# Kernel optimization log

Hardware: AMD Instinct MI355X
Metric: run time of the kernel (lower is better)

The kernel has to match this reference:

```python
import jax, jax.numpy as jnp
import numpy as np

B, N, C_IN, F, OUT = 32, 1000, 128, 128, 64
RATIOS = (0.8, 0.8)


def setup_inputs() -> dict:
    key = jax.random.key(0)
    ks = jax.random.split(key, 10)
    N_nodes = jax.random.randint(ks[0], (B,), 500, N + 1, dtype=jnp.int32)
    ar = jnp.arange(N)
    mask = (ar[None, :] < N_nodes[:, None]).astype(jnp.float32)  # [B,N]
    A = (jax.random.uniform(ks[1], (B, N, N)) < 0.02).astype(jnp.float32)
    A = A * (1.0 - jnp.eye(N, dtype=jnp.float32))
    A = jnp.maximum(A, A.transpose(0, 2, 1))  # symmetric, no self loops
    A = A * mask[:, :, None] * mask[:, None, :]
    x = jax.random.normal(ks[2], (B, N, C_IN)) * mask[..., None]

    def lin(k, fin, fout):
        bnd = 1.0 / np.sqrt(fin)
        kw, kb = jax.random.split(k)
        W = jax.random.uniform(kw, (fout, fin), minval=-bnd, maxval=bnd)
        b = jax.random.uniform(kb, (fout,), minval=-bnd, maxval=bnd)
        return W, b

    W0, b0 = lin(ks[3], C_IN, F)
    W1, b1 = lin(ks[4], F, F)
    W2, b2 = lin(ks[5], F, F)
    bnd = 1.0 / np.sqrt(F)
    p0 = jax.random.uniform(ks[6], (F, 1), minval=-bnd, maxval=bnd)
    p1 = jax.random.uniform(ks[7], (F, 1), minval=-bnd, maxval=bnd)
    Wfc, bfc = lin(ks[8], F, OUT)
    return dict(x=x, A=A, mask=mask, N_nodes=N_nodes,
                W0=W0, b0=b0, W1=W1, b1=b1, W2=W2, b2=b2,
                p0=p0, p1=p1, Wfc=Wfc, bfc=bfc)


def _gconv(x, A, mask, W, b):
    # K=1 Kipf-Welling conv: L = D^-1/2 (A+I) D^-1/2; relu(Linear(L x)) * mask
    n = A.shape[1]
    A_hat = A + jnp.eye(n, dtype=A.dtype)
    D = (jnp.sum(A_hat, axis=1) + 1e-5) ** -0.5  # [B,N]
    L = D[:, :, None] * A_hat * D[:, None, :]
    h = jnp.einsum('bij,bjc->bic', L, x)
    h = h @ W.T + b
    return jax.nn.relu(h) * mask[..., None]


def _pool(x, A, mask, N_nodes, p, ratio):
    # score each node, drop the N_remove lowest-scoring valid nodes per graph
    y = (x @ p)[..., 0] / jnp.sqrt(jnp.sum(p ** 2))  # [B,N]
    N_remove = (N_nodes.astype(jnp.float32) * (1.0 - ratio)).astype(jnp.int32)
    y_key = jnp.where(mask > 0, y, jnp.inf)  # invalid nodes rank last
    ranks = jnp.argsort(jnp.argsort(y_key, axis=1), axis=1)  # ascending rank
    new_mask = ((ranks >= N_remove[:, None]) & (mask > 0)).astype(x.dtype)
    x = x * jnp.tanh(y)[..., None] * new_mask[..., None]
    A = new_mask[:, :, None] * A * new_mask[:, None, :]
    return x, A, new_mask, N_nodes - N_remove


def reference(x, A, mask, N_nodes, W0, b0, W1, b1, W2, b2, p0, p1, Wfc, bfc):
    h = _gconv(x, A, mask, W0, b0)
    h, A1, m1, n1 = _pool(h, A, mask, N_nodes, p0, RATIOS[0])
    h = _gconv(h, A1, m1, W1, b1)
    h, A2, m2, n2 = _pool(h, A1, m1, n1, p1, RATIOS[1])
    h = _gconv(h, A2, m2, W2, b2)
    g = jnp.max(h, axis=1)  # [B,F] global max pool
    return g @ Wfc.T + bfc  # [B,OUT]
```

## Files before the change

### kernel.cpp

```cpp
#include <hip/hip_runtime.h>
#include <math.h>

#define BB 32
#define NN 1000
#define CC 128
#define FF 128
#define OO 64
#define CAP 128
#define NB 40

#define RMC ((float)(1.0 - 0.8))


__global__ void k_csr(const float* __restrict__ A, const float* __restrict__ mask,
                      const int* __restrict__ Nn,
                      const float* __restrict__ p0, const float* __restrict__ p1,
                      const float* __restrict__ W0, const float* __restrict__ W1,
                      const float* __restrict__ W2,
                      short* __restrict__ idx, int* __restrict__ cnt,
                      float* __restrict__ D, float* __restrict__ dg,
                      float* __restrict__ m, float* __restrict__ gate,
                      int* __restrict__ ncur0, float* __restrict__ pn,
                      float* __restrict__ Wt){
  int blk = blockIdx.x, lane = threadIdx.x;
  int r8 = blk & 7, t = blk >> 3;
  int b = r8 + 8*(t/1001), i = t % 1001;
  if (i == NN){
    for (int j = lane; j < NN; j += 64){
      float v = mask[b*NN + j]; m[b*NN + j] = v; gate[b*NN + j] = v;
    }
    if (lane == 0) ncur0[b] = Nn[b];
    if (b == 0 && lane == 1){ float s=0.f; for(int c=0;c<FF;c++) s += p0[c]*p0[c]; pn[0] = sqrtf(s); }
    if (b == 1 && lane == 1){ float s=0.f; for(int c=0;c<FF;c++) s += p1[c]*p1[c]; pn[1] = sqrtf(s); }
    for (int e = b*1536 + lane; e < (b+1)*1536; e += 64){
      int s = e / (FF*CC), rem = e % (FF*CC);
      int c = rem >> 7, f = rem & 127;
      const float* W = (s == 0) ? W0 : (s == 1) ? W1 : W2;
      Wt[(size_t)s*FF*CC + rem] = W[f*CC + c];
    }
    return;
  }
  if (mask[b*NN + i] == 0.f){
    if (lane == 0){
      cnt[b*NN + i] = 0;
      D[b*NN + i]  = 1.0f / sqrtf(1.0f + 1e-5f);
      dg[b*NN + i] = 0.f;
    }
    return;
  }
  const float4* row = (const float4*)(A + ((size_t)b*NN + i)*NN);
  short* out = idx + ((size_t)b*NN + i)*CAP;
  int count = 0;
  for (int base = 0; base < 250; base += 64){
    int q = base + lane;
    float4 v;
    if (q < 250) v = row[q]; else { v.x=v.y=v.z=v.w=0.f; }
    int lc = (v.x!=0.f) + (v.y!=0.f) + (v.z!=0.f) + (v.w!=0.f);
    int pre = lc;
    #pragma unroll
    for (int off = 1; off < 64; off <<= 1){
      int t2 = __shfl_up(pre, off);
      if (lane >= off) pre += t2;
    }
    int tot = __shfl(pre, 63);
    pre -= lc;
    int slot = count + pre;
    int j = q*4;
    if (v.x!=0.f && slot < CAP) out[slot++] = (short)j;
    if (v.y!=0.f && slot < CAP) out[slot++] = (short)(j+1);
    if (v.z!=0.f && slot < CAP) out[slot++] = (short)(j+2);
    if (v.w!=0.f && slot < CAP) out[slot++] = (short)(j+3);
    count += tot;
  }
  if (lane == 0){
    int cn = (count < CAP) ? count : CAP;
    cnt[b*NN + i] = cn;
    float Dv = 1.0f / sqrtf((float)cn + 1.0f + 1e-5f);
    D[b*NN + i]  = Dv;
    dg[b*NN + i] = Dv;
  }
}

__global__ void k_agglin(const short* __restrict__ idx, const int* __restrict__ cnt,
                         const float* __restrict__ D, const float* __restrict__ dg,
                         const float* __restrict__ m, const float* __restrict__ gate,
                         const float* __restrict__ h,
                         const float* __restrict__ Wt,
                         const float* __restrict__ bias, float* __restrict__ Hout){
  __shared__ float t[NB][CC];
  __shared__ int   nb[8][CAP];
  __shared__ float dn[8][CAP];
  int blk = blockIdx.x, tid = threadIdx.x;
  int r8 = blk & 7, tq = blk >> 3;
  int b = r8 + 8*(tq/25);
  int i0 = (tq % 25) * NB;
  int w = tid >> 6, lane = tid & 63;
  int g = lane >> 5, l32 = lane & 31;
  const float* hb = h + (size_t)b*NN*CC;
  int*   nbw = nb[w];
  float* dnw = dn[w];
  for (int q = 0; q < 5; q++){
    int lr = q*8 + w;
    int i  = i0 + lr;
    if (m[b*NN + i] == 0.f){
      if (g == 0){ float4 z = {0.f,0.f,0.f,0.f}; *(float4*)&t[lr][l32<<2] = z; }
      continue;
    }
    int n = cnt[b*NN + i];
    const short* r = idx + ((size_t)b*NN + i)*CAP;
    int j0 = 0; float d0 = 0.f; bool k0 = false;
    if (lane < n){ j0 = (int)r[lane]; d0 = dg[b*NN + j0]; k0 = (d0 != 0.f); }
    unsigned long long bal = __ballot(k0);
    int pre = __popcll(bal & ((1ull << lane) - 1ull));
    if (k0){ nbw[pre] = j0*CC; dnw[pre] = d0; }
    int nlive = __popcll(bal);
    if (n > 64){
      int e = lane + 64; int j1 = 0; float d1 = 0.f; bool k1 = false;
      if (e < n){ j1 = (int)r[e]; d1 = dg[b*NN + j1]; k1 = (d1 != 0.f); }
      unsigned long long bal1 = __ballot(k1);
      int pre1 = __popcll(bal1 & ((1ull << lane) - 1ull));
      if (k1){ nbw[nlive + pre1] = j1*CC; dnw[nlive + pre1] = d1; }
      nlive += __popcll(bal1);
    }
    int np = (nlive + 15) & ~15;
    if (lane < np - nlive){ nbw[nlive + lane] = 0; dnw[nlive + lane] = 0.f; }
    __builtin_amdgcn_wave_barrier();
    float4 a0 = {0.f,0.f,0.f,0.f}, a1 = a0, a2 = a0, a3 = a0;
    for (int k = 0; k < np; k += 16){
      int e = k + g;
      float4 v0 = *(const float4*)(hb + nbw[e   ] + (l32<<2));
      float4 v1 = *(const float4*)(hb + nbw[e+ 2] + (l32<<2));
      float4 v2 = *(const float4*)(hb + nbw[e+ 4] + (l32<<2));
      float4 v3 = *(const float4*)(hb + nbw[e+ 6] + (l32<<2));
      float4 v4 = *(const float4*)(hb + nbw[e+ 8] + (l32<<2));
      float4 v5 = *(const float4*)(hb + nbw[e+10] + (l32<<2));
      float4 v6 = *(const float4*)(hb + nbw[e+12] + (l32<<2));
      float4 v7 = *(const float4*)(hb + nbw[e+14] + (l32<<2));
      float e0 = dnw[e], e1 = dnw[e+2], e2 = dnw[e+4], e3 = dnw[e+6];
      float e4 = dnw[e+8], e5 = dnw[e+10], e6 = dnw[e+12], e7 = dnw[e+14];
      a0.x += e0*v0.x; a0.y += e0*v0.y; a0.z += e0*v0.z; a0.w += e0*v0.w;
      a1.x += e1*v1.x; a1.y += e1*v1.y; a1.z += e1*v1.z; a1.w += e1*v1.w;
      a2.x += e2*v2.x; a2.y += e2*v2.y; a2.z += e2*v2.z; a2.w += e2*v2.w;
      a3.x += e3*v3.x; a3.y += e3*v3.y; a3.z += e3*v3.z; a3.w += e3*v3.w;
      a0.x += e4*v4.x; a0.y += e4*v4.y; a0.z += e4*v4.z; a0.w += e4*v4.w;
      a1.x += e5*v5.x; a1.y += e5*v5.y; a1.z += e5*v5.z; a1.w += e5*v5.w;
      a2.x += e6*v6.x; a2.y += e6*v6.y; a2.z += e6*v6.z; a2.w += e6*v6.w;
      a3.x += e7*v7.x; a3.y += e7*v7.y; a3.z += e7*v7.z; a3.w += e7*v7.w;
    }
    float4 Y;
    Y.x = (a0.x + a1.x) + (a2.x + a3.x);
    Y.y = (a0.y + a1.y) + (a2.y + a3.y);
    Y.z = (a0.z + a1.z) + (a2.z + a3.z);
    Y.w = (a0.w + a1.w) + (a2.w + a3.w);
    Y.x += __shfl_xor(Y.x, 32);
    Y.y += __shfl_xor(Y.y, 32);
    Y.z += __shfl_xor(Y.z, 32);
    Y.w += __shfl_xor(Y.w, 32);
    float Di = D[b*NN + i];
    float gi = gate[b*NN + i];
    if (g == 0){
      float4 hv = *(const float4*)(hb + (size_t)i*CC + (l32<<2));
      float4 o;
      o.x = Di*Y.x + Di*Di*(gi*hv.x);
      o.y = Di*Y.y + Di*Di*(gi*hv.y);
      o.z = Di*Y.z + Di*Di*(gi*hv.z);
      o.w = Di*Y.w + Di*Di*(gi*hv.w);
      *(float4*)&t[lr][l32<<2] = o;
    }
  }
  __syncthreads();
  if (tid < 256){
    int fg = tid & 31;
    int nr = tid >> 5;
    float acc[5][4];
    float4 bi = ((const float4*)bias)[fg];
    #pragma unroll
    for (int n5 = 0; n5 < 5; n5++){
      acc[n5][0]=bi.x; acc[n5][1]=bi.y; acc[n5][2]=bi.z; acc[n5][3]=bi.w;
    }
    for (int c4 = 0; c4 < 32; c4++){
      float4 tv[5];
      #pragma unroll
      for (int n5 = 0; n5 < 5; n5++)
        tv[n5] = *((const float4*)&t[nr + n5*8][c4*4]);
      #pragma unroll
      for (int k = 0; k < 4; k++){
        float4 wv = ((const float4*)Wt)[(size_t)(c4*4 + k)*32 + fg];
        #pragma unroll
        for (int n5 = 0; n5 < 5; n5++){
          float tvv = (k==0) ? tv[n5].x : (k==1) ? tv[n5].y : (k==2) ? tv[n5].z : tv[n5].w;
          acc[n5][0] += tvv*wv.x; acc[n5][1] += tvv*wv.y;
          acc[n5][2] += tvv*wv.z; acc[n5][3] += tvv*wv.w;
        }
      }
    }
    #pragma unroll
    for (int n5 = 0; n5 < 5; n5++){
      int i = i0 + nr + n5*8;
      float mi = m[b*NN + i];
      float4 o4;
      o4.x = fmaxf(acc[n5][0], 0.f)*mi;
      o4.y = fmaxf(acc[n5][1], 0.f)*mi;
      o4.z = fmaxf(acc[n5][2], 0.f)*mi;
      o4.w = fmaxf(acc[n5][3], 0.f)*mi;
      ((float4*)&Hout[((size_t)b*NN + i)*CC])[fg] = o4;
    }
  }
}

__global__ void k_score(const float* __restrict__ H, const float* __restrict__ p,
                        const float* __restrict__ pn, float* __restrict__ y){
  int blk = blockIdx.x, lane = threadIdx.x;
  int r8 = blk & 7, t = blk >> 3;
  int b = r8 + 8*(t/1000), i = t % 1000;
  const float* hrow = H + ((size_t)b*NN + i)*CC;
  float s = hrow[lane]*p[lane] + hrow[lane+64]*p[lane+64];
  for (int off = 32; off > 0; off >>= 1) s += __shfl_down(s, off);
  if (lane == 0) y[b*NN + i] = s / pn[0];
}

__global__ void k_pool(const float* __restrict__ y, float* __restrict__ m,
                       const int* __restrict__ ncur_in, int* __restrict__ ncur_out,
                       float* __restrict__ gate){
  __shared__ float yk[NN];
  int blk = blockIdx.x, tid = threadIdx.x;
  int r8 = blk & 7, t = blk >> 3;
  int b = r8 + 8*(t >> 2), xx = t & 3;
  int i = xx*256 + tid;
  for (int j = tid; j < NN; j += 256)
    yk[j] = (m[b*NN + j] > 0.f) ? y[b*NN + j] : INFINITY;
  __syncthreads();
  int n = ncur_in[b];
  int nr = (int)((float)n * RMC);
  float myv = (i < NN) ? yk[i] : INFINITY;
  int cnt = 0;
  const float4* yk4 = (const float4*)yk;
  #pragma unroll 5
  for (int q = 0; q < 250; q++){
    float4 v = yk4[q];
    int j0 = q*4;
    cnt += (int)((v.x < myv) || (v.x == myv && j0     < i));
    cnt += (int)((v.y < myv) || (v.y == myv && j0 + 1 < i));
    cnt += (int)((v.z < myv) || (v.z == myv && j0 + 2 < i));
    cnt += (int)((v.w < myv) || (v.w == myv && j0 + 3 < i));
  }
  if (i < NN){
    bool keep = (cnt >= nr) && (m[b*NN + i] > 0.f);
    m[b*NN + i]    = keep ? 1.0f : 0.0f;
    gate[b*NN + i] = keep ? tanhf(y[b*NN + i]) : 0.0f;
  }
  if (xx == 0 && tid == 0) ncur_out[b] = n - nr;
}

__global__ void k_deg(const short* __restrict__ idx, const int* __restrict__ cnt,
                      const float* __restrict__ m, const float* __restrict__ gate,
                      float* __restrict__ D, float* __restrict__ dg){
  __shared__ float ml[NN];
  int blk = blockIdx.x, tid = threadIdx.x;
  int r8 = blk & 7, t = blk >> 3;
  int b = r8 + 8*(t >> 2), xx = t & 3;
  for (int i = tid; i < NN; i += 256) ml[i] = m[b*NN + i];
  __syncthreads();
  int j = xx*250 + tid;
  if (tid < 250){
    const short* r = idx + ((size_t)b*NN + j)*CAP;
    int n = cnt[b*NN + j];
    float s0=0.f, s1=0.f, s2=0.f, s3=0.f;
    int k = 0;
    for (; k+4 <= n; k += 4){
      s0 += ml[r[k]]; s1 += ml[r[k+1]]; s2 += ml[r[k+2]]; s3 += ml[r[k+3]];
    }
    for (; k < n; k++) s0 += ml[r[k]];
    float Dv = 1.0f / sqrtf(((s0+s1)+(s2+s3)) + 1.0f + 1e-5f);
    D[b*NN + j]  = Dv;
    dg[b*NN + j] = Dv * gate[b*NN + j];
  }
}

__global__ void k_fmax(const float* __restrict__ H, const float* __restrict__ m,
                       float* __restrict__ part){
  int blk = blockIdx.x, c = threadIdx.x;
  int r8 = blk & 7, t = blk >> 3;
  int b = r8 + 8*(t >> 3), sx = t & 7;
  float mx = 0.f;
  int i0 = sx*125;
  for (int i = i0; i < i0+125; i++){
    if (m[b*NN + i] != 0.f)
      mx = fmaxf(mx, H[((size_t)b*NN + i)*CC + c]);
  }
  part[((size_t)b*8 + sx)*CC + c] = mx;
}

__global__ void k_fc(const float* __restrict__ part, const float* __restrict__ Wfc,
                     const float* __restrict__ bfc, float* __restrict__ out){
  __shared__ float g[FF];
  int b = blockIdx.x, tid = threadIdx.x;
  float mx = 0.f;
  #pragma unroll
  for (int s = 0; s < 8; s++) mx = fmaxf(mx, part[((size_t)b*8 + s)*CC + tid]);
  g[tid] = mx;
  __syncthreads();
  if (tid < OO){
    float acc = bfc[tid];
    for (int c = 0; c < FF; c++) acc += g[c]*Wfc[tid*FF + c];
    out[b*OO + tid] = acc;
  }
}

extern "C" void kernel_launch(void* const* d_in, const int* in_sizes, int n_in,
                              void* d_out, int out_size, void* d_ws, size_t ws_size,
                              hipStream_t stream) {
  const float* x    = (const float*)d_in[0];
  const float* A    = (const float*)d_in[1];
  const float* mask = (const float*)d_in[2];
  const int*   Nn   = (const int*)  d_in[3];
  const float* W0   = (const float*)d_in[4];
  const float* b0   = (const float*)d_in[5];
  const float* W1   = (const float*)d_in[6];
  const float* b1   = (const float*)d_in[7];
  const float* W2   = (const float*)d_in[8];
  const float* b2   = (const float*)d_in[9];
  const float* p0   = (const float*)d_in[10];
  const float* p1   = (const float*)d_in[11];
  const float* Wfc  = (const float*)d_in[12];
  const float* bfc  = (const float*)d_in[13];
  float* out = (float*)d_out;

  char* w = (char*)d_ws;
  float* H   = (float*)w; w += (size_t)BB*NN*CC*4;
  float* H2  = (float*)w; w += (size_t)BB*NN*CC*4;
  short* idx = (short*)w; w += (size_t)BB*NN*CAP*2;
  float* Wt  = (float*)w; w += (size_t)3*FF*CC*4;
  float* part= (float*)w; w += (size_t)8*BB*CC*4;
  int*   cnt = (int*)w;   w += (size_t)BB*NN*4;
  float* D   = (float*)w; w += (size_t)BB*NN*4;
  float* m   = (float*)w; w += (size_t)BB*NN*4;
  float* ysc = (float*)w; w += (size_t)BB*NN*4;
  float* gate= (float*)w; w += (size_t)BB*NN*4;
  float* dg  = (float*)w; w += (size_t)BB*NN*4;
  int*   ncur= (int*)w;   w += 3*BB*sizeof(int);
  float* pn  = (float*)w; w += 64;

  k_csr<<<32032, 64, 0, stream>>>(A, mask, Nn, p0, p1, W0, W1, W2,
                                  idx, cnt, D, dg, m, gate, ncur, pn, Wt);

  k_agglin<<<800, 512, 0, stream>>>(idx, cnt, D, dg, m, gate, x,
                                    Wt + 0*FF*CC, b0, H);
  k_score<<<32000, 64, 0, stream>>>(H, p0, pn + 0, ysc);
  k_pool<<<128, 256, 0, stream>>>(ysc, m, ncur + 0*BB, ncur + 1*BB, gate);
  k_deg<<<128, 256, 0, stream>>>(idx, cnt, m, gate, D, dg);

  k_agglin<<<800, 512, 0, stream>>>(idx, cnt, D, dg, m, gate, H,
                                    Wt + 1*FF*CC, b1, H2);
  k_score<<<32000, 64, 0, stream>>>(H2, p1, pn + 1, ysc);
  k_pool<<<128, 256, 0, stream>>>(ysc, m, ncur + 1*BB, ncur + 2*BB, gate);
  k_deg<<<128, 256, 0, stream>>>(idx, cnt, m, gate, D, dg);

  k_agglin<<<800, 512, 0, stream>>>(idx, cnt, D, dg, m, gate, H2,
                                    Wt + 2*FF*CC, b2, H);

  k_fmax<<<256, 128, 0, stream>>>(H, m, part);
  k_fc<<<BB, 128, 0, stream>>>(part, Wfc, bfc, out);
}
```

Before: 442.9 us.

## Split aggregation from linear and stage 16-channel feature slices in LDS

The fused aggregate+linear kernel is split into two kernels. The new aggregation kernel loads a 16-channel slice of every node's features for one graph into shared memory (64KB) and gathers neighbours from LDS rather than global memory. It writes its result to a new intermediate buffer T, which a separate linear kernel then reads. This trades scattered global gathers for LDS gathers and an extra full-size intermediate round trip plus more kernel launches. Each block also reloads the whole graph slice although it only handles a quarter of the rows.

After: 616.5 us. +39.2%, slower.

```diff
diff --git a/kernel.cpp b/kernel.cpp
--- a/kernel.cpp
+++ b/kernel.cpp
@@ -81,130 +81,125 @@
   }
 }
 
-__global__ void k_agglin(const short* __restrict__ idx, const int* __restrict__ cnt,
-                         const float* __restrict__ D, const float* __restrict__ dg,
-                         const float* __restrict__ m, const float* __restrict__ gate,
-                         const float* __restrict__ h,
-                         const float* __restrict__ Wt,
-                         const float* __restrict__ bias, float* __restrict__ Hout){
-  __shared__ float t[NB][CC];
+__global__ void k_aggc(const short* __restrict__ idx, const int* __restrict__ cnt,
+                       const float* __restrict__ D, const float* __restrict__ dg,
+                       const float* __restrict__ m, const float* __restrict__ gate,
+                       const float* __restrict__ h, float* __restrict__ T){
+  __shared__ float hs[NN*16];
   __shared__ int   nb[8][CAP];
   __shared__ float dn[8][CAP];
   int blk = blockIdx.x, tid = threadIdx.x;
-  int r8 = blk & 7, tq = blk >> 3;
-  int b = r8 + 8*(tq/25);
-  int i0 = (tq % 25) * NB;
+  int r8 = blk & 7;
+  int b  = r8 + 8*((blk >> 3) & 3);
+  int ck = (blk >> 5) & 7;
+  int rq = blk >> 8;
+  int c0 = ck*16;
   int w = tid >> 6, lane = tid & 63;
-  int g = lane >> 5, l32 = lane & 31;
+  int c = lane & 15, s = lane >> 4;
   const float* hb = h + (size_t)b*NN*CC;
   int*   nbw = nb[w];
   float* dnw = dn[w];
-  for (int q = 0; q < 5; q++){
-    int lr = q*8 + w;
-    int i  = i0 + lr;
-    if (m[b*NN + i] == 0.f){
-      if (g == 0){ float4 z = {0.f,0.f,0.f,0.f}; *(float4*)&t[lr][l32<<2] = z; }
+  {
+    const float* src = hb + c0;
+    float4* hs4 = (float4*)hs;
+    for (int q = tid; q < NN*4; q += 512){
+      int row = q >> 2, f4 = q & 3;
+      hs4[q] = *(const float4*)(src + (size_t)row*CC + f4*4);
+    }
+  }
+  __syncthreads();
+  for (int rr = w; rr < 250; rr += 8){
+    int ib = rq*250 + rr;
+    if (m[b*NN + ib] == 0.f){
+      if (s == 0) T[((size_t)b*NN + ib)*CC + c0 + c] = 0.f;
       continue;
     }
-    int n = cnt[b*NN + i];
-    const short* r = idx + ((size_t)b*NN + i)*CAP;
+    int n = cnt[b*NN + ib];
+    const short* r = idx + ((size_t)b*NN + ib)*CAP;
     int j0 = 0; float d0 = 0.f; bool k0 = false;
     if (lane < n){ j0 = (int)r[lane]; d0 = dg[b*NN + j0]; k0 = (d0 != 0.f); }
     unsigned long long bal = __ballot(k0);
     int pre = __popcll(bal & ((1ull << lane) - 1ull));
-    if (k0){ nbw[pre] = j0*CC; dnw[pre] = d0; }
+    if (k0){ nbw[pre] = j0*16; dnw[pre] = d0; }
     int nlive = __popcll(bal);
     if (n > 64){
       int e = lane + 64; int j1 = 0; float d1 = 0.f; bool k1 = false;
       if (e < n){ j1 = (int)r[e]; d1 = dg[b*NN + j1]; k1 = (d1 != 0.f); }
       unsigned long long bal1 = __ballot(k1);
       int pre1 = __popcll(bal1 & ((1ull << lane) - 1ull));
-      if (k1){ nbw[nlive + pre1] = j1*CC; dnw[nlive + pre1] = d1; }
+      if (k1){ nbw[nlive + pre1] = j1*16; dnw[nlive + pre1] = d1; }
       nlive += __popcll(bal1);
     }
-    int np = (nlive + 15) & ~15;
+    int np = (nlive + 7) & ~7;
     if (lane < np - nlive){ nbw[nlive + lane] = 0; dnw[nlive + lane] = 0.f; }
     __builtin_amdgcn_wave_barrier();
-    float4 a0 = {0.f,0.f,0.f,0.f}, a1 = a0, a2 = a0, a3 = a0;
-    for (int k = 0; k < np; k += 16){
-      int e = k + g;
-      float4 v0 = *(const float4*)(hb + nbw[e   ] + (l32<<2));
-      float4 v1 = *(const float4*)(hb + nbw[e+ 2] + (l32<<2));
-      float4 v2 = *(const float4*)(hb + nbw[e+ 4] + (l32<<2));
-      float4 v3 = *(const float4*)(hb + nbw[e+ 6] + (l32<<2));
-      float4 v4 = *(const float4*)(hb + nbw[e+ 8] + (l32<<2));
-      float4 v5 = *(const float4*)(hb + nbw[e+10] + (l32<<2));
-      float4 v6 = *(const float4*)(hb + nbw[e+12] + (l32<<2));
-      float4 v7 = *(const float4*)(hb + nbw[e+14] + (l32<<2));
-      float e0 = dnw[e], e1 = dnw[e+2], e2 = dnw[e+4], e3 = dnw[e+6];
-      float e4 = dnw[e+8], e5 = dnw[e+10], e6 = dnw[e+12], e7 = dnw[e+14];
-      a0.x += e0*v0.x; a0.y += e0*v0.y; a0.z += e0*v0.z; a0.w += e0*v0.w;
-      a1.x += e1*v1.x; a1.y += e1*v1.y; a1.z += e1*v1.z; a1.w += e1*v1.w;
-      a2.x += e2*v2.x; a2.y += e2*v2.y; a2.z += e2*v2.z; a2.w += e2*v2.w;
-      a3.x += e3*v3.x; a3.y += e3*v3.y; a3.z += e3*v3.z; a3.w += e3*v3.w;
-      a0.x += e4*v4.x; a0.y += e4*v4.y; a0.z += e4*v4.z; a0.w += e4*v4.w;
-      a1.x += e5*v5.x; a1.y += e5*v5.y; a1.z += e5*v5.z; a1.w += e5*v5.w;
-      a2.x += e6*v6.x; a2.y += e6*v6.y; a2.z += e6*v6.z; a2.w += e6*v6.w;
-      a3.x += e7*v7.x; a3.y += e7*v7.y; a3.z += e7*v7.z; a3.w += e7*v7.w;
-    }
-    float4 Y;
-    Y.x = (a0.x + a1.x) + (a2.x + a3.x);
-    Y.y = (a0.y + a1.y) + (a2.y + a3.y);
-    Y.z = (a0.z + a1.z) + (a2.z + a3.z);
-    Y.w = (a0.w + a1.w) + (a2.w + a3.w);
-    Y.x += __shfl_xor(Y.x, 32);
-    Y.y += __shfl_xor(Y.y, 32);
-    Y.z += __shfl_xor(Y.z, 32);
-    Y.w += __shfl_xor(Y.w, 32);
-    float Di = D[b*NN + i];
-    float gi = gate[b*NN + i];
-    if (g == 0){
-      float4 hv = *(const float4*)(hb + (size_t)i*CC + (l32<<2));
-      float4 o;
-      o.x = Di*Y.x + Di*Di*(gi*hv.x);
-      o.y = Di*Y.y + Di*Di*(gi*hv.y);
-      o.z = Di*Y.z + Di*Di*(gi*hv.z);
-      o.w = Di*Y.w + Di*Di*(gi*hv.w);
-      *(float4*)&t[lr][l32<<2] = o;
-    }
-  }
-  __syncthreads();
-  if (tid < 256){
-    int fg = tid & 31;
-    int nr = tid >> 5;
-    float acc[5][4];
-    float4 bi = ((const float4*)bias)[fg];
+    float bA = 0.f, bB = 0.f;
+    for (int k = 0; k < np; k += 8){
+      float dA = dnw[k + s],     hA = hs[nbw[k + s]     + c];
+      float dB = dnw[k + s + 4], hB = hs[nbw[k + s + 4] + c];
+      bA += dA*hA;
+      bB += dB*hB;
+    }
+    float u  = bA + __shfl_xor(bA, 32);
+    float v  = bB + __shfl_xor(bB, 32);
+    float e2 = u + v;
+    float Y  = e2 + __shfl_xor(e2, 16);
+    float Di = D[b*NN + ib];
+    float gi = gate[b*NN + ib];
+    if (s == 0){
+      float hv = hs[ib*16 + c];
+      T[((size_t)b*NN + ib)*CC + c0 + c] = Di*Y + Di*Di*(gi*hv);
+    }
+  }
+}
+
+__global__ void k_lin(const float* __restrict__ T, const float* __restrict__ m,
+                      const float* __restrict__ Wt,
+                      const float* __restrict__ bias, float* __restrict__ Hout){
+  __shared__ float t[NB][CC];
+  int blk = blockIdx.x, tid = threadIdx.x;
+  int r8 = blk & 7, tq = blk >> 3;
+  int b = r8 + 8*(tq/25);
+  int i0 = (tq % 25) * NB;
+  const float4* Tg = (const float4*)(T + ((size_t)b*NN + i0)*CC);
+  float4* tl = (float4*)&t[0][0];
+  #pragma unroll
+  for (int e = 0; e < 5; e++) tl[tid + e*256] = Tg[tid + e*256];
+  __syncthreads();
+  int fg = tid & 31;
+  int nr = tid >> 5;
+  float acc[5][4];
+  float4 bi = ((const float4*)bias)[fg];
+  #pragma unroll
+  for (int n5 = 0; n5 < 5; n5++){
+    acc[n5][0]=bi.x; acc[n5][1]=bi.y; acc[n5][2]=bi.z; acc[n5][3]=bi.w;
+  }
+  for (int c4 = 0; c4 < 32; c4++){
+    float4 tv[5];
     #pragma unroll
-    for (int n5 = 0; n5 < 5; n5++){
-      acc[n5][0]=bi.x; acc[n5][1]=bi.y; acc[n5][2]=bi.z; acc[n5][3]=bi.w;
-    }
-    for (int c4 = 0; c4 < 32; c4++){
-      float4 tv[5];
+    for (int n5 = 0; n5 < 5; n5++)
+      tv[n5] = *((const float4*)&t[nr + n5*8][c4*4]);
+    #pragma unroll
+    for (int k = 0; k < 4; k++){
+      float4 wv = ((const float4*)Wt)[(size_t)(c4*4 + k)*32 + fg];
       #pragma unroll
-      for (int n5 = 0; n5 < 5; n5++)
-        tv[n5] = *((const float4*)&t[nr + n5*8][c4*4]);
-      #pragma unroll
-      for (int k = 0; k < 4; k++){
-        float4 wv = ((const float4*)Wt)[(size_t)(c4*4 + k)*32 + fg];
-        #pragma unroll
-        for (int n5 = 0; n5 < 5; n5++){
-          float tvv = (k==0) ? tv[n5].x : (k==1) ? tv[n5].y : (k==2) ? tv[n5].z : tv[n5].w;
-          acc[n5][0] += tvv*wv.x; acc[n5][1] += tvv*wv.y;
-          acc[n5][2] += tvv*wv.z; acc[n5][3] += tvv*wv.w;
-        }
+      for (int n5 = 0; n5 < 5; n5++){
+        float tvv = (k==0) ? tv[n5].x : (k==1) ? tv[n5].y : (k==2) ? tv[n5].z : tv[n5].w;
+        acc[n5][0] += tvv*wv.x; acc[n5][1] += tvv*wv.y;
+        acc[n5][2] += tvv*wv.z; acc[n5][3] += tvv*wv.w;
       }
     }
-    #pragma unroll
-    for (int n5 = 0; n5 < 5; n5++){
-      int i = i0 + nr + n5*8;
-      float mi = m[b*NN + i];
-      float4 o4;
-      o4.x = fmaxf(acc[n5][0], 0.f)*mi;
-      o4.y = fmaxf(acc[n5][1], 0.f)*mi;
-      o4.z = fmaxf(acc[n5][2], 0.f)*mi;
-      o4.w = fmaxf(acc[n5][3], 0.f)*mi;
-      ((float4*)&Hout[((size_t)b*NN + i)*CC])[fg] = o4;
-    }
+  }
+  #pragma unroll
+  for (int n5 = 0; n5 < 5; n5++){
+    int i = i0 + nr + n5*8;
+    float mi = m[b*NN + i];
+    float4 o4;
+    o4.x = fmaxf(acc[n5][0], 0.f)*mi;
+    o4.y = fmaxf(acc[n5][1], 0.f)*mi;
+    o4.z = fmaxf(acc[n5][2], 0.f)*mi;
+    o4.w = fmaxf(acc[n5][3], 0.f)*mi;
+    ((float4*)&Hout[((size_t)b*NN + i)*CC])[fg] = o4;
   }
 }
 
@@ -329,6 +324,7 @@
   char* w = (char*)d_ws;
   float* H   = (float*)w; w += (size_t)BB*NN*CC*4;
   float* H2  = (float*)w; w += (size_t)BB*NN*CC*4;
+  float* T   = (float*)w; w += (size_t)BB*NN*CC*4;
   short* idx = (short*)w; w += (size_t)BB*NN*CAP*2;
   float* Wt  = (float*)w; w += (size_t)3*FF*CC*4;
   float* part= (float*)w; w += (size_t)8*BB*CC*4;
@@ -344,20 +340,20 @@
   k_csr<<<32032, 64, 0, stream>>>(A, mask, Nn, p0, p1, W0, W1, W2,
                                   idx, cnt, D, dg, m, gate, ncur, pn, Wt);
 
-  k_agglin<<<800, 512, 0, stream>>>(idx, cnt, D, dg, m, gate, x,
-                                    Wt + 0*FF*CC, b0, H);
+  k_aggc<<<1024, 512, 0, stream>>>(idx, cnt, D, dg, m, gate, x, T);
+  k_lin<<<800, 256, 0, stream>>>(T, m, Wt + 0*FF*CC, b0, H);
   k_score<<<32000, 64, 0, stream>>>(H, p0, pn + 0, ysc);
   k_pool<<<128, 256, 0, stream>>>(ysc, m, ncur + 0*BB, ncur + 1*BB, gate);
   k_deg<<<128, 256, 0, stream>>>(idx, cnt, m, gate, D, dg);
 
-  k_agglin<<<800, 512, 0, stream>>>(idx, cnt, D, dg, m, gate, H,
-                                    Wt + 1*FF*CC, b1, H2);
+  k_aggc<<<1024, 512, 0, stream>>>(idx, cnt, D, dg, m, gate, H, T);
+  k_lin<<<800, 256, 0, stream>>>(T, m, Wt + 1*FF*CC, b1, H2);
   k_score<<<32000, 64, 0, stream>>>(H2, p1, pn + 1, ysc);
   k_pool<<<128, 256, 0, stream>>>(ysc, m, ncur + 1*BB, ncur + 2*BB, gate);
   k_deg<<<128, 256, 0, stream>>>(idx, cnt, m, gate, D, dg);
 
-  k_agglin<<<800, 512, 0, stream>>>(idx, cnt, D, dg, m, gate, H2,
-                                    Wt + 2*FF*CC, b2, H);
+  k_aggc<<<1024, 512, 0, stream>>>(idx, cnt, D, dg, m, gate, H2, T);
+  k_lin<<<800, 256, 0, stream>>>(T, m, Wt + 2*FF*CC, b2, H);
 
   k_fmax<<<256, 128, 0, stream>>>(H, m, part);
   k_fc<<<BB, 128, 0, stream>>>(part, Wfc, bfc, out);
```
